# Kernel tuning notes

Measured on AMD Instinct MI355X. Metric: run time of the kernel, lower is better.

The kernel has to match this reference:

```python
import jax, jax.numpy as jnp
import numpy as np

N_NODES = 100000
N_EDGES = 1600000
N_QUERY = 500000
F_IN, HID, EMB = 7, 128, 64


def _glorot(key, fan_in, fan_out):
    lim = float(np.sqrt(6.0 / (fan_in + fan_out)))
    return jax.random.uniform(key, (fan_in, fan_out), jnp.float32, -lim, lim)


def setup_inputs() -> dict:
    key = jax.random.key(0)
    ks = jax.random.split(key, 16)
    x = jax.random.normal(ks[0], (N_NODES, F_IN), jnp.float32)
    edge_index = jax.random.randint(ks[1], (2, N_EDGES), 0, N_NODES, jnp.int64)
    query_edges = jax.random.randint(ks[2], (2, N_QUERY), 0, N_NODES, jnp.int64)
    return {
        "x": x,
        "edge_index": edge_index,
        "query_edges": query_edges,
        # GCN layer 1 / 2
        "W1": _glorot(ks[3], F_IN, HID), "b1": jnp.zeros((HID,), jnp.float32),
        "W2": _glorot(ks[4], HID, HID), "b2": jnp.zeros((HID,), jnp.float32),
        # encoder fc
        "Wfc": _glorot(ks[5], HID, EMB), "bfc": jnp.zeros((EMB,), jnp.float32),
        # decoder MLP
        "Wd1": _glorot(ks[6], 2 * EMB, HID), "bd1": jnp.zeros((HID,), jnp.float32),
        "Wd2": _glorot(ks[7], HID, HID // 2), "bd2": jnp.zeros((HID // 2,), jnp.float32),
        "Wd3": _glorot(ks[8], HID // 2, 1), "bd3": jnp.zeros((1,), jnp.float32),
    }


def _gcn_conv(x, W, b, src, dst, n_nodes):
    """PyG GCNConv: add self-loops + symmetric deg^{-1/2} normalization."""
    h = x @ W  # [N, F_out]
    deg = jnp.ones((n_nodes,), h.dtype).at[dst].add(jnp.ones_like(dst, h.dtype))  # +1 self-loop
    dinv = jax.lax.rsqrt(deg)
    norm = dinv[src] * dinv[dst]  # [E]
    agg = jnp.zeros_like(h).at[dst].add(h[src] * norm[:, None])  # scatter-add messages
    agg = agg + h * (dinv * dinv)[:, None]  # self-loop contribution
    return agg + b


def reference(x, edge_index, query_edges, W1, b1, W2, b2, Wfc, bfc, Wd1, bd1, Wd2, bd2, Wd3, bd3):
    n = x.shape[0]
    src, dst = edge_index[0], edge_index[1]
    # encoder (eval mode: dropout = identity)
    h = jax.nn.relu(_gcn_conv(x, W1, b1, src, dst, n))
    h = jax.nn.relu(_gcn_conv(h, W2, b2, src, dst, n))
    z = h @ Wfc + bfc  # [N, EMB]
    # pair gather + MLP decode
    zc = jnp.concatenate([z[query_edges[0]], z[query_edges[1]]], axis=-1)  # [Q, 2*EMB]
    d = jax.nn.relu(zc @ Wd1 + bd1)
    d = jax.nn.relu(d @ Wd2 + bd2)
    logits = (d @ Wd3 + bd3).squeeze(-1)  # [Q]
    return jax.nn.sigmoid(logits)
```

## Files before the change

### kernel.cpp

```cpp
#include <hip/hip_runtime.h>
#include <hip/hip_bf16.h>
#include <cstdint>
#include <cstddef>

constexpr int TPB = 256;
constexpr int SCAN_B = 1024;
constexpr int NB   = 128;
constexpr int BSH  = 10;
constexpr int NPB  = 1 << BSH;
constexpr int EPB  = 4096;
using bf16x8 = __attribute__((ext_vector_type(8))) short;
using f32x4  = __attribute__((ext_vector_type(4))) float;

static inline int cdiv(int a, int b) { return (a + b - 1) / b; }

__device__ __forceinline__ float bf2f(short u) {
  return __uint_as_float(((unsigned int)(unsigned short)u) << 16);
}
__device__ __forceinline__ short f2bf(float f) {
  unsigned int u = __float_as_uint(f);
  return (short)((u + 0x7FFF + ((u >> 16) & 1)) >> 16);
}


__global__ __launch_bounds__(256)
void bucket_hist_kernel(const int* __restrict__ dst, int* __restrict__ bh,
                        int e_cnt, int n_blk) {
  __shared__ int h[NB];
  int tid = threadIdx.x;
  if (tid < NB) h[tid] = 0;
  __syncthreads();
  int base = blockIdx.x * EPB;
  for (int i = tid; i < EPB; i += TPB) {
    int e = base + i;
    if (e < e_cnt) atomicAdd(&h[dst[e] >> BSH], 1);
  }
  __syncthreads();
  if (tid < NB) bh[tid * n_blk + blockIdx.x] = h[tid];
}

__global__ __launch_bounds__(SCAN_B)
void scan_block_kernel(const int* __restrict__ counts, int* __restrict__ rowptr,
                       int* __restrict__ bsum, int n) {
  __shared__ int wsum[16];
  const int tid = threadIdx.x;
  const int i = blockIdx.x * SCAN_B + tid;
  const int lane = tid & 63;
  const int w = tid >> 6;
  int v = (i < n) ? counts[i] : 0;
  int s = v;
  #pragma unroll
  for (int off = 1; off < 64; off <<= 1) {
    int t = __shfl_up(s, off, 64);
    if (lane >= off) s += t;
  }
  if (lane == 63) wsum[w] = s;
  __syncthreads();
  if (tid < 16) {
    int ws_ = wsum[tid];
    #pragma unroll
    for (int off = 1; off < 16; off <<= 1) {
      int t = __shfl_up(ws_, off, 64);
      if (tid >= off) ws_ += t;
    }
    wsum[tid] = ws_;
  }
  __syncthreads();
  int woff = (w == 0) ? 0 : wsum[w - 1];
  if (i < n) rowptr[i] = woff + s - v;
  if (tid == SCAN_B - 1) bsum[blockIdx.x] = woff + s;
}

__global__ __launch_bounds__(256)
void scan_fin_kernel(int* __restrict__ rowptr, const int* __restrict__ bsum,
                     int nb, int n, int total) {
  __shared__ int sb[128];
  int tid = threadIdx.x;
  if (tid == 0) {
    int run = 0;
    for (int b = 0; b < nb; ++b) { sb[b] = run; run += bsum[b]; }
  }
  __syncthreads();
  int i = blockIdx.x * TPB + tid;
  if (i < n) rowptr[i] += sb[i / SCAN_B];
  if (i == 0) rowptr[n] = total;
}

__global__ __launch_bounds__(256)
void bucket_scatter_kernel(const int* __restrict__ src, const int* __restrict__ dst,
                           const int* __restrict__ eoff, unsigned int* __restrict__ ebuf,
                           int e_cnt, int n_blk) {
  __shared__ int cur[NB];
  int tid = threadIdx.x;
  if (tid < NB) cur[tid] = eoff[tid * n_blk + blockIdx.x];
  __syncthreads();
  int base = blockIdx.x * EPB;
  for (int i = tid; i < EPB; i += TPB) {
    int e = base + i;
    if (e < e_cnt) {
      int d = dst[e];
      int b = d >> BSH;
      int pos = atomicAdd(&cur[b], 1);
      ebuf[pos] = ((unsigned int)src[e] << BSH) | (unsigned int)(d & (NPB - 1));
    }
  }
}

__global__ __launch_bounds__(256)
void node_hist_kernel(const unsigned int* __restrict__ ebuf, const int* __restrict__ eoff,
                      int* __restrict__ counts, float* __restrict__ dinv,
                      int n_blk, int n_nodes) {
  __shared__ int nh[NPB];
  int b = blockIdx.x;
  for (int i = threadIdx.x; i < NPB; i += TPB) nh[i] = 0;
  __syncthreads();
  int wb = eoff[b * n_blk];
  int we = eoff[(b + 1) * n_blk];
  for (int i = wb + threadIdx.x; i < we; i += TPB)
    atomicAdd(&nh[ebuf[i] & (NPB - 1)], 1);
  __syncthreads();
  int nbase = b << BSH;
  for (int i = threadIdx.x; i < NPB; i += TPB) {
    int node = nbase + i;
    if (node < n_nodes) {
      counts[node] = nh[i];
      dinv[node] = rsqrtf((float)nh[i] + 1.0f);
    }
  }
}

__global__ __launch_bounds__(256)
void final_scatter_kernel(const unsigned int* __restrict__ ebuf, const int* __restrict__ eoff,
                          const int* __restrict__ rowptr, int* __restrict__ csr_src,
                          int n_blk, int n_nodes) {
  __shared__ int cur[NPB];
  int b = blockIdx.x;
  int nbase = b << BSH;
  for (int i = threadIdx.x; i < NPB; i += TPB) {
    int node = nbase + i;
    cur[i] = (node < n_nodes) ? rowptr[node] : 0;
  }
  __syncthreads();
  int wb = eoff[b * n_blk];
  int we = eoff[(b + 1) * n_blk];
  for (int i = wb + threadIdx.x; i < we; i += TPB) {
    unsigned int p = ebuf[i];
    int pos = atomicAdd(&cur[p & (NPB - 1)], 1);
    csr_src[pos] = (int)(p >> BSH);
  }
}


__global__ void pad_x8_kernel(const float* __restrict__ x, float* __restrict__ x8, int n) {
  int i = blockIdx.x * TPB + threadIdx.x;
  if (i >= n * 8) return;
  int node = i >> 3, f = i & 7;
  x8[i] = (f < 7) ? x[node * 7 + f] : 0.0f;
}

__global__ __launch_bounds__(256)
void prep_weights_kernel(const float* __restrict__ W1, const float* __restrict__ W2,
                         const float* __restrict__ Wfc, const float* __restrict__ bfc,
                         const float* __restrict__ Wd1, const float* __restrict__ bd1,
                         float* __restrict__ W1p, unsigned short* __restrict__ W2T,
                         unsigned short* __restrict__ WcaT, unsigned short* __restrict__ WcbT,
                         float* __restrict__ bca, float* __restrict__ bcb) {
  int b = blockIdx.x;
  int tid = threadIdx.x;
  if (b == 0) {
    for (int i = tid; i < 8 * 128; i += TPB)
      W1p[i] = (i < 7 * 128) ? W1[i] : 0.0f;
    int j = tid & 127;
    int which = tid >> 7;
    float acc = which ? 0.0f : bd1[j];
    int mo = which ? 64 : 0;
    #pragma unroll 8
    for (int m = 0; m < 64; ++m) acc = fmaf(bfc[m], Wd1[(mo + m) * 128 + j], acc);
    if (which) bcb[j] = acc; else bca[j] = acc;
  } else if (b <= 64) {
    int idx = (b - 1) * 256 + tid;
    int n = idx >> 7, k = idx & 127;
    W2T[idx] = (unsigned short)f2bf(W2[k * 128 + n]);
  } else {
    int idx = (b - 65) * 256 + tid;
    int j = idx >> 7, k = idx & 127;
    float accA = 0.0f, accB = 0.0f;
    #pragma unroll 8
    for (int m = 0; m < 64; ++m) {
      float w = Wfc[k * 64 + m];
      accA = fmaf(w, Wd1[m * 128 + j], accA);
      accB = fmaf(w, Wd1[(64 + m) * 128 + j], accB);
    }
    WcaT[j * 128 + k] = (unsigned short)f2bf(accA);
    WcbT[j * 128 + k] = (unsigned short)f2bf(accB);
  }
}


__global__ __launch_bounds__(256)
void agg_x_kernel(const int* __restrict__ rowptr, const int* __restrict__ csr_src,
                  const float* __restrict__ dinv, const float* __restrict__ x8,
                  float* __restrict__ aggx, int n_nodes) {
  int gid = blockIdx.x * TPB + threadIdx.x;
  int node = gid >> 3;
  int f = gid & 7;
  if (node >= n_nodes) return;
  float dn = dinv[node];
  float acc0 = x8[(size_t)node * 8 + f] * dn * dn;
  float acc1 = 0.0f;
  int beg = rowptr[node], end = rowptr[node + 1];
  int i = beg;
  for (; i + 1 < end; i += 2) {
    int s0 = csr_src[i];
    int s1 = csr_src[i + 1];
    float w0 = dinv[s0] * dn;
    float w1 = dinv[s1] * dn;
    acc0 = fmaf(x8[(size_t)s0 * 8 + f], w0, acc0);
    acc1 = fmaf(x8[(size_t)s1 * 8 + f], w1, acc1);
  }
  if (i < end) {
    int s = csr_src[i];
    acc0 = fmaf(x8[(size_t)s * 8 + f], dinv[s] * dn, acc0);
  }
  aggx[(size_t)node * 8 + f] = acc0 + acc1;
}

__global__ __launch_bounds__(256)
void gather4_kernel(const int* __restrict__ rowptr, const int* __restrict__ csr_src,
                    const float* __restrict__ dinv, const uint4* __restrict__ h1s,
                    uint4* __restrict__ g1, int n_nodes) {
  int wid = (blockIdx.x * TPB + threadIdx.x) >> 6;
  if (wid >= n_nodes) return;
  int lane = threadIdx.x & 63;
  int qtr = lane >> 4;
  int l = lane & 15;
  float acc[8];
  #pragma unroll
  for (int j = 0; j < 8; ++j) acc[j] = 0.0f;
  auto addv = [&](uint4 v) {
    unsigned int u[4] = {v.x, v.y, v.z, v.w};
    #pragma unroll
    for (int p = 0; p < 4; ++p) {
      acc[2 * p]     += __uint_as_float(u[p] << 16);
      acc[2 * p + 1] += __uint_as_float(u[p] & 0xffff0000u);
    }
  };
  if (qtr == 0) addv(h1s[(size_t)wid * 16 + l]);
  int beg = rowptr[wid], end = rowptr[wid + 1];
  int i = beg + qtr;
  for (; i + 4 < end; i += 8) {
    int s0 = csr_src[i];
    int s1 = csr_src[i + 4];
    uint4 v0 = h1s[(size_t)s0 * 16 + l];
    uint4 v1 = h1s[(size_t)s1 * 16 + l];
    addv(v0);
    addv(v1);
  }
  if (i < end) addv(h1s[(size_t)csr_src[i] * 16 + l]);
  #pragma unroll
  for (int j = 0; j < 8; ++j) {
    acc[j] += __shfl_xor(acc[j], 16, 64);
    acc[j] += __shfl_xor(acc[j], 32, 64);
  }
  if (qtr == 0) {
    float dn = dinv[wid];
    unsigned int w[4];
    #pragma unroll
    for (int p = 0; p < 4; ++p) {
      unsigned int lo = (unsigned int)(unsigned short)f2bf(acc[2 * p] * dn);
      unsigned int hi = (unsigned int)(unsigned short)f2bf(acc[2 * p + 1] * dn);
      w[p] = lo | (hi << 16);
    }
    uint4 o; o.x = w[0]; o.y = w[1]; o.z = w[2]; o.w = w[3];
    g1[(size_t)wid * 16 + l] = o;
  }
}

template<int K, int CO>
__global__ __launch_bounds__(256)
void mm_tiled(const float* __restrict__ in, const float* __restrict__ W,
              const float* __restrict__ bias, const float* __restrict__ scale,
              unsigned short* __restrict__ outv, int n_rows) {
  constexpr int BM = 64;
  constexpr int BK = K;
  constexpr int SS = BK + 1 + (BK & 1);
  constexpr int TM = 4;
  constexpr int TN = CO / 16;
  __shared__ float s_in[BM][SS];
  __shared__ float s_w[BK][CO];
  const int tid = threadIdx.x;
  const int base = blockIdx.x * BM;
  const int tr = tid >> 4;
  const int tc = tid & 15;

  float acc[TM][TN];
  #pragma unroll
  for (int m = 0; m < TM; ++m)
    #pragma unroll
    for (int n = 0; n < TN; ++n) acc[m][n] = 0.0f;

  {
    constexpr int F4 = BM * (BK / 4);
    #pragma unroll
    for (int t = tid; t < F4; t += TPB) {
      int r = t / (BK / 4), c4 = t % (BK / 4);
      int row = base + r;
      float4 v = make_float4(0.f, 0.f, 0.f, 0.f);
      if (row < n_rows) v = *(const float4*)(in + (size_t)row * K + c4 * 4);
      s_in[r][c4 * 4 + 0] = v.x;
      s_in[r][c4 * 4 + 1] = v.y;
      s_in[r][c4 * 4 + 2] = v.z;
      s_in[r][c4 * 4 + 3] = v.w;
    }
    constexpr int WF4 = BK * CO / 4;
    #pragma unroll
    for (int t = tid; t < WF4; t += TPB)
      *(float4*)(&s_w[0][0] + t * 4) = *(const float4*)(W + t * 4);
  }
  __syncthreads();

  #pragma unroll
  for (int kk = 0; kk < BK; ++kk) {
    float a[TM], b[TN];
    #pragma unroll
    for (int m = 0; m < TM; ++m) a[m] = s_in[tr * TM + m][kk];
    #pragma unroll
    for (int n = 0; n < TN; ++n) b[n] = s_w[kk][tc + 16 * n];
    #pragma unroll
    for (int m = 0; m < TM; ++m)
      #pragma unroll
      for (int n = 0; n < TN; ++n) acc[m][n] = fmaf(a[m], b[n], acc[m][n]);
  }

  #pragma unroll
  for (int m = 0; m < TM; ++m) {
    int row = base + tr * TM + m;
    if (row < n_rows) {
      float sc = scale[row];
      #pragma unroll
      for (int n = 0; n < TN; ++n) {
        int j = tc + 16 * n;
        float v = fmaxf(acc[m][n] + bias[j], 0.0f) * sc;
        outv[(size_t)row * CO + j] = (unsigned short)f2bf(v);
      }
    }
  }
}

template<int K, int N>
__global__ __launch_bounds__(256)
void mm_mfma(const unsigned short* __restrict__ A, const unsigned short* __restrict__ WT,
             const float* __restrict__ bias, unsigned short* __restrict__ out,
             int n_rows, int do_relu) {
  constexpr int KS = K / 32;
  constexpr int NT = N / 16;
  const int lane = threadIdx.x & 63;
  const int col = lane & 15;
  const int sub = lane >> 4;
  const int wid = threadIdx.x >> 6;

  bf16x8 bfrag[KS][NT];
  #pragma unroll
  for (int ks = 0; ks < KS; ++ks)
    #pragma unroll
    for (int nt = 0; nt < NT; ++nt)
      bfrag[ks][nt] = *(const bf16x8*)(WT + (size_t)(nt * 16 + col) * K + ks * 32 + sub * 8);
  float bv[NT];
  #pragma unroll
  for (int nt = 0; nt < NT; ++nt) bv[nt] = bias ? bias[nt * 16 + col] : 0.0f;

  int ntiles = (n_rows + 15) >> 4;
  int stride = gridDim.x * 4;
  for (int tile = blockIdx.x * 4 + wid; tile < ntiles; tile += stride) {
    int row_a = tile * 16 + col;
    if (row_a >= n_rows) row_a = n_rows - 1;
    bf16x8 afrag[KS];
    #pragma unroll
    for (int ks = 0; ks < KS; ++ks)
      afrag[ks] = *(const bf16x8*)(A + (size_t)row_a * K + ks * 32 + sub * 8);
    f32x4 acc[NT];
    #pragma unroll
    for (int nt = 0; nt < NT; ++nt) acc[nt] = {0.f, 0.f, 0.f, 0.f};
    #pragma unroll
    for (int ks = 0; ks < KS; ++ks)
      #pragma unroll
      for (int nt = 0; nt < NT; ++nt)
        acc[nt] = __builtin_amdgcn_mfma_f32_16x16x32_bf16(afrag[ks], bfrag[ks][nt], acc[nt], 0, 0, 0);
    #pragma unroll
    for (int r = 0; r < 4; ++r) {
      int ro = tile * 16 + sub * 4 + r;
      if (ro < n_rows) {
        #pragma unroll
        for (int nt = 0; nt < NT; ++nt) {
          float v = acc[nt][r] + bv[nt];
          if (do_relu) v = fmaxf(v, 0.0f);
          out[(size_t)ro * N + nt * 16 + col] = (unsigned short)f2bf(v);
        }
      }
    }
  }
}

__global__ __launch_bounds__(256)
void decoder_mfma_kernel(const int* __restrict__ qsrc, const int* __restrict__ qdst,
                         const unsigned short* __restrict__ atab,
                         const unsigned short* __restrict__ btab,
                         const float* __restrict__ Wd2, const float* __restrict__ bd2,
                         const float* __restrict__ Wd3, const float* __restrict__ bd3,
                         float* __restrict__ out, int n_query) {
  const int lane = threadIdx.x & 63;
  const int col = lane & 15;
  const int sub = lane >> 4;

  bf16x8 bfrag[4][4];
  #pragma unroll
  for (int ks = 0; ks < 4; ++ks)
    #pragma unroll
    for (int nt = 0; nt < 4; ++nt) {
      bf16x8 f;
      #pragma unroll
      for (int j = 0; j < 8; ++j) {
        int k = ks * 32 + sub * 8 + j;
        int n = nt * 16 + col;
        f[j] = f2bf(Wd2[k * 64 + n]);
      }
      bfrag[ks][nt] = f;
    }
  float bd2v[4], wd3v[4];
  #pragma unroll
  for (int nt = 0; nt < 4; ++nt) {
    bd2v[nt] = bd2[nt * 16 + col];
    wd3v[nt] = Wd3[nt * 16 + col];
  }
  const float bd3s = bd3[0];

  int wave = (blockIdx.x * TPB + threadIdx.x) >> 6;
  int nwaves = gridDim.x * (TPB / 64);
  int ntiles = (n_query + 15) >> 4;
  for (int t = wave; t < ntiles; t += nwaves) {
    int qb = t << 4;
    int q = qb + col;
    if (q >= n_query) q = n_query - 1;
    int si = qsrc[q], di = qdst[q];
    const bf16x8* ar = (const bf16x8*)(atab + (size_t)si * 128);
    const bf16x8* br = (const bf16x8*)(btab + (size_t)di * 128);
    bf16x8 afrag[4];
    #pragma unroll
    for (int ks = 0; ks < 4; ++ks) {
      bf16x8 av = ar[ks * 4 + sub];
      bf16x8 bv = br[ks * 4 + sub];
      bf16x8 d;
      #pragma unroll
      for (int j = 0; j < 8; ++j)
        d[j] = f2bf(fmaxf(bf2f(av[j]) + bf2f(bv[j]), 0.0f));
      afrag[ks] = d;
    }
    f32x4 acc[4];
    #pragma unroll
    for (int nt = 0; nt < 4; ++nt) acc[nt] = {0.f, 0.f, 0.f, 0.f};
    #pragma unroll
    for (int ks = 0; ks < 4; ++ks)
      #pragma unroll
      for (int nt = 0; nt < 4; ++nt)
        acc[nt] = __builtin_amdgcn_mfma_f32_16x16x32_bf16(afrag[ks], bfrag[ks][nt], acc[nt], 0, 0, 0);
    float part[4] = {0.f, 0.f, 0.f, 0.f};
    #pragma unroll
    for (int nt = 0; nt < 4; ++nt)
      #pragma unroll
      for (int r = 0; r < 4; ++r) {
        float v = fmaxf(acc[nt][r] + bd2v[nt], 0.0f);
        part[r] = fmaf(v, wd3v[nt], part[r]);
      }
    #pragma unroll
    for (int off = 1; off < 16; off <<= 1)
      #pragma unroll
      for (int r = 0; r < 4; ++r) part[r] += __shfl_xor(part[r], off, 64);
    if (col == 0) {
      int row0 = qb + sub * 4;
      #pragma unroll
      for (int r = 0; r < 4; ++r) {
        int qq = row0 + r;
        if (qq < n_query) out[qq] = 1.0f / (1.0f + __expf(-(part[r] + bd3s)));
      }
    }
  }
}

extern "C" void kernel_launch(void* const* d_in, const int* in_sizes, int n_in,
                              void* d_out, int out_size, void* d_ws, size_t ws_size,
                              hipStream_t stream) {
  const float* x    = (const float*)d_in[0];
  const int*   ei   = (const int*)d_in[1];
  const int*   qe   = (const int*)d_in[2];
  const float* W1   = (const float*)d_in[3];
  const float* b1   = (const float*)d_in[4];
  const float* W2   = (const float*)d_in[5];
  const float* b2   = (const float*)d_in[6];
  const float* Wfc  = (const float*)d_in[7];
  const float* bfc  = (const float*)d_in[8];
  const float* Wd1  = (const float*)d_in[9];
  const float* bd1  = (const float*)d_in[10];
  const float* Wd2  = (const float*)d_in[11];
  const float* bd2  = (const float*)d_in[12];
  const float* Wd3  = (const float*)d_in[13];
  const float* bd3  = (const float*)d_in[14];
  float* out = (float*)d_out;

  const int n_nodes = in_sizes[0] / 7;
  const int n_edges = in_sizes[1] / 2;
  const int n_query = in_sizes[2] / 2;
  const int* e_src = ei;
  const int* e_dst = ei + n_edges;
  const int* q_src = qe;
  const int* q_dst = qe + n_query;

  const int n_blk1 = cdiv(n_edges, EPB);
  const int bh_len = NB * n_blk1;
  const int n_bucket = cdiv(n_nodes, NPB);

  char* wp = (char*)d_ws;
  auto take = [&](size_t bytes) { char* p = wp; wp += (bytes + 255) & ~size_t(255); return p; };
  float* dinv    = (float*)take((size_t)n_nodes * 4);
  int*   counts  = (int*)  take((size_t)n_nodes * 4);
  int*   rowptr  = (int*)  take((size_t)(n_nodes + 1) * 4);
  int*   bsum    = (int*)  take(512 * 4);
  int*   bh      = (int*)  take((size_t)(bh_len + 1) * 4);
  int*   eoff    = (int*)  take((size_t)(bh_len + 1) * 4);
  unsigned int* ebuf = (unsigned int*)take((size_t)n_edges * 4);
  int*   csr_src = (int*)  take((size_t)n_edges * 4);
  float* x8      = (float*)take((size_t)n_nodes * 8 * 4);
  float* aggx    = (float*)take((size_t)n_nodes * 8 * 4);
  float* W1p     = (float*)take(8 * 128 * 4);
  unsigned short* W2T   = (unsigned short*)take(128 * 128 * 2);
  unsigned short* WcaT  = (unsigned short*)take(128 * 128 * 2);
  unsigned short* WcbT  = (unsigned short*)take(128 * 128 * 2);
  float* bca     = (float*)take(128 * 4);
  float* bcb     = (float*)take(128 * 4);
  float* bufP    = (float*)take((size_t)n_nodes * 128 * 4);
  float* bufQ    = (float*)take((size_t)n_nodes * 128 * 4);
  float* bufR    = (float*)take((size_t)n_nodes * 64 * 4);

  const int mm_blocks = cdiv(n_nodes, 64);
  const int node_blocks = cdiv(n_nodes, TPB);
  const int scan_blocks = cdiv(n_nodes, SCAN_B);
  const int escan_blocks = cdiv(bh_len, SCAN_B);
  const int mfma_blocks = min(1024, cdiv(cdiv(n_nodes, 16), 4));

  bucket_hist_kernel<<<n_blk1, TPB, 0, stream>>>(e_dst, bh, n_edges, n_blk1);
  scan_block_kernel<<<escan_blocks, SCAN_B, 0, stream>>>(bh, eoff, bsum, bh_len);
  scan_fin_kernel<<<cdiv(bh_len, TPB), TPB, 0, stream>>>(eoff, bsum, escan_blocks, bh_len, n_edges);
  bucket_scatter_kernel<<<n_blk1, TPB, 0, stream>>>(e_src, e_dst, eoff, ebuf, n_edges, n_blk1);
  node_hist_kernel<<<n_bucket, TPB, 0, stream>>>(ebuf, eoff, counts, dinv, n_blk1, n_nodes);
  scan_block_kernel<<<scan_blocks, SCAN_B, 0, stream>>>(counts, rowptr, bsum, n_nodes);
  scan_fin_kernel<<<node_blocks, TPB, 0, stream>>>(rowptr, bsum, scan_blocks, n_nodes, n_edges);
  final_scatter_kernel<<<n_bucket, TPB, 0, stream>>>(ebuf, eoff, rowptr, csr_src, n_blk1, n_nodes);

  pad_x8_kernel<<<cdiv(n_nodes * 8, TPB), TPB, 0, stream>>>(x, x8, n_nodes);
  prep_weights_kernel<<<129, TPB, 0, stream>>>(W1, W2, Wfc, bfc, Wd1, bd1,
                                               W1p, W2T, WcaT, WcbT, bca, bcb);

  agg_x_kernel<<<cdiv(n_nodes * 8, TPB), TPB, 0, stream>>>(rowptr, csr_src, dinv, x8, aggx, n_nodes);
  mm_tiled<8, 128><<<mm_blocks, TPB, 0, stream>>>(aggx, W1p, b1, dinv, (unsigned short*)bufP, n_nodes);

  gather4_kernel<<<cdiv(n_nodes * 64, TPB), TPB, 0, stream>>>(rowptr, csr_src, dinv,
                                                              (const uint4*)bufP, (uint4*)bufQ, n_nodes);
  mm_mfma<128, 128><<<mfma_blocks, TPB, 0, stream>>>((const unsigned short*)bufQ, W2T, b2,
                                                     (unsigned short*)bufP, n_nodes, 1);

  unsigned short* atab = (unsigned short*)bufQ;
  unsigned short* btab = (unsigned short*)bufR;
  mm_mfma<128, 128><<<mfma_blocks, TPB, 0, stream>>>((const unsigned short*)bufP, WcaT, bca,
                                                     atab, n_nodes, 0);
  mm_mfma<128, 128><<<mfma_blocks, TPB, 0, stream>>>((const unsigned short*)bufP, WcbT, bcb,
                                                     btab, n_nodes, 0);

  decoder_mfma_kernel<<<2048, TPB, 0, stream>>>(q_src, q_dst, atab, btab, Wd2, bd2, Wd3, bd3, out, n_query);
}
```

Before: 306.0 us.

## Fuse layer-2 neighbor gather with W2 MFMA matmul; drop x padding kernel

Replaces the separate layer-2 gather kernel and its MFMA matmul with one fused kernel. Each block aggregates 64 nodes into shared-memory bf16 rows, then multiplies them by W2 (staged in padded LDS) using MFMA. This avoids writing and re-reading the intermediate aggregated features through global memory and saves a kernel launch. The pad_x8 kernel is also removed, with agg_x reading the unpadded 7-wide x directly. Each wave now processes 16 nodes serially, and the per-block W2 staging lowers parallelism and may reduce occupancy.

Measured after the change: 370.6 us. +21.1%, slower.

```diff
diff --git a/kernel.cpp b/kernel.cpp
--- a/kernel.cpp
+++ b/kernel.cpp
@@ -9,6 +9,7 @@
 constexpr int BSH  = 10;
 constexpr int NPB  = 1 << BSH;
 constexpr int EPB  = 4096;
+constexpr int LP   = 136;
 using bf16x8 = __attribute__((ext_vector_type(8))) short;
 using f32x4  = __attribute__((ext_vector_type(4))) float;
 
@@ -150,13 +151,6 @@
   }
 }
 
-
-__global__ void pad_x8_kernel(const float* __restrict__ x, float* __restrict__ x8, int n) {
-  int i = blockIdx.x * TPB + threadIdx.x;
-  if (i >= n * 8) return;
-  int node = i >> 3, f = i & 7;
-  x8[i] = (f < 7) ? x[node * 7 + f] : 0.0f;
-}
 
 __global__ __launch_bounds__(256)
 void prep_weights_kernel(const float* __restrict__ W1, const float* __restrict__ W2,
@@ -199,14 +193,15 @@
 
 __global__ __launch_bounds__(256)
 void agg_x_kernel(const int* __restrict__ rowptr, const int* __restrict__ csr_src,
-                  const float* __restrict__ dinv, const float* __restrict__ x8,
+                  const float* __restrict__ dinv, const float* __restrict__ x,
                   float* __restrict__ aggx, int n_nodes) {
   int gid = blockIdx.x * TPB + threadIdx.x;
   int node = gid >> 3;
   int f = gid & 7;
   if (node >= n_nodes) return;
+  bool live = (f < 7);
   float dn = dinv[node];
-  float acc0 = x8[(size_t)node * 8 + f] * dn * dn;
+  float acc0 = live ? x[(size_t)node * 7 + f] * dn * dn : 0.0f;
   float acc1 = 0.0f;
   int beg = rowptr[node], end = rowptr[node + 1];
   int i = beg;
@@ -215,65 +210,16 @@
     int s1 = csr_src[i + 1];
     float w0 = dinv[s0] * dn;
     float w1 = dinv[s1] * dn;
-    acc0 = fmaf(x8[(size_t)s0 * 8 + f], w0, acc0);
-    acc1 = fmaf(x8[(size_t)s1 * 8 + f], w1, acc1);
-  }
-  if (i < end) {
+    if (live) {
+      acc0 = fmaf(x[(size_t)s0 * 7 + f], w0, acc0);
+      acc1 = fmaf(x[(size_t)s1 * 7 + f], w1, acc1);
+    }
+  }
+  if (i < end && live) {
     int s = csr_src[i];
-    acc0 = fmaf(x8[(size_t)s * 8 + f], dinv[s] * dn, acc0);
+    acc0 = fmaf(x[(size_t)s * 7 + f], dinv[s] * dn, acc0);
   }
   aggx[(size_t)node * 8 + f] = acc0 + acc1;
-}
-
-__global__ __launch_bounds__(256)
-void gather4_kernel(const int* __restrict__ rowptr, const int* __restrict__ csr_src,
-                    const float* __restrict__ dinv, const uint4* __restrict__ h1s,
-                    uint4* __restrict__ g1, int n_nodes) {
-  int wid = (blockIdx.x * TPB + threadIdx.x) >> 6;
-  if (wid >= n_nodes) return;
-  int lane = threadIdx.x & 63;
-  int qtr = lane >> 4;
-  int l = lane & 15;
-  float acc[8];
-  #pragma unroll
-  for (int j = 0; j < 8; ++j) acc[j] = 0.0f;
-  auto addv = [&](uint4 v) {
-    unsigned int u[4] = {v.x, v.y, v.z, v.w};
-    #pragma unroll
-    for (int p = 0; p < 4; ++p) {
-      acc[2 * p]     += __uint_as_float(u[p] << 16);
-      acc[2 * p + 1] += __uint_as_float(u[p] & 0xffff0000u);
-    }
-  };
-  if (qtr == 0) addv(h1s[(size_t)wid * 16 + l]);
-  int beg = rowptr[wid], end = rowptr[wid + 1];
-  int i = beg + qtr;
-  for (; i + 4 < end; i += 8) {
-    int s0 = csr_src[i];
-    int s1 = csr_src[i + 4];
-    uint4 v0 = h1s[(size_t)s0 * 16 + l];
-    uint4 v1 = h1s[(size_t)s1 * 16 + l];
-    addv(v0);
-    addv(v1);
-  }
-  if (i < end) addv(h1s[(size_t)csr_src[i] * 16 + l]);
-  #pragma unroll
-  for (int j = 0; j < 8; ++j) {
-    acc[j] += __shfl_xor(acc[j], 16, 64);
-    acc[j] += __shfl_xor(acc[j], 32, 64);
-  }
-  if (qtr == 0) {
-    float dn = dinv[wid];
-    unsigned int w[4];
-    #pragma unroll
-    for (int p = 0; p < 4; ++p) {
-      unsigned int lo = (unsigned int)(unsigned short)f2bf(acc[2 * p] * dn);
-      unsigned int hi = (unsigned int)(unsigned short)f2bf(acc[2 * p + 1] * dn);
-      w[p] = lo | (hi << 16);
-    }
-    uint4 o; o.x = w[0]; o.y = w[1]; o.z = w[2]; o.w = w[3];
-    g1[(size_t)wid * 16 + l] = o;
-  }
 }
 
 template<int K, int CO>
@@ -342,6 +288,98 @@
         int j = tc + 16 * n;
         float v = fmaxf(acc[m][n] + bias[j], 0.0f) * sc;
         outv[(size_t)row * CO + j] = (unsigned short)f2bf(v);
+      }
+    }
+  }
+}
+
+__global__ __launch_bounds__(256)
+void gcn_fused_kernel(const int* __restrict__ rowptr, const int* __restrict__ csr_src,
+                      const float* __restrict__ dinv, const uint4* __restrict__ h1s,
+                      const unsigned short* __restrict__ W2T, const float* __restrict__ b2,
+                      unsigned short* __restrict__ h2, int n_nodes) {
+  __shared__ unsigned short g1s[64 * LP];
+  __shared__ unsigned short w2s[128 * LP];
+  const int tid = threadIdx.x;
+  for (int i = tid; i < 128 * 16; i += TPB) {
+    int row = i >> 4, seg = i & 15;
+    *(uint4*)&w2s[row * LP + seg * 8] = *(const uint4*)(W2T + (size_t)row * 128 + seg * 8);
+  }
+  __syncthreads();
+
+  const int lane = tid & 63;
+  const int w = tid >> 6;
+  const int qtr = lane >> 4;
+  const int l = lane & 15;
+  const int base = blockIdx.x * 64;
+
+  for (int nn = 0; nn < 16; ++nn) {
+    int node = base + w * 16 + nn;
+    if (node >= n_nodes) break;
+    float acc[8];
+    #pragma unroll
+    for (int j = 0; j < 8; ++j) acc[j] = 0.0f;
+    auto addv = [&](uint4 v) {
+      unsigned int u[4] = {v.x, v.y, v.z, v.w};
+      #pragma unroll
+      for (int p = 0; p < 4; ++p) {
+        acc[2 * p]     += __uint_as_float(u[p] << 16);
+        acc[2 * p + 1] += __uint_as_float(u[p] & 0xffff0000u);
+      }
+    };
+    if (qtr == 0) addv(h1s[(size_t)node * 16 + l]);
+    int beg = rowptr[node], end = rowptr[node + 1];
+    int i = beg + qtr;
+    for (; i + 4 < end; i += 8) {
+      int s0 = csr_src[i];
+      int s1 = csr_src[i + 4];
+      uint4 v0 = h1s[(size_t)s0 * 16 + l];
+      uint4 v1 = h1s[(size_t)s1 * 16 + l];
+      addv(v0);
+      addv(v1);
+    }
+    if (i < end) addv(h1s[(size_t)csr_src[i] * 16 + l]);
+    #pragma unroll
+    for (int j = 0; j < 8; ++j) {
+      acc[j] += __shfl_xor(acc[j], 16, 64);
+      acc[j] += __shfl_xor(acc[j], 32, 64);
+    }
+    if (qtr == 0) {
+      float dn = dinv[node];
+      unsigned int wv[4];
+      #pragma unroll
+      for (int p = 0; p < 4; ++p) {
+        unsigned int lo = (unsigned int)(unsigned short)f2bf(acc[2 * p] * dn);
+        unsigned int hi = (unsigned int)(unsigned short)f2bf(acc[2 * p + 1] * dn);
+        wv[p] = lo | (hi << 16);
+      }
+      uint4 o; o.x = wv[0]; o.y = wv[1]; o.z = wv[2]; o.w = wv[3];
+      *(uint4*)&g1s[(w * 16 + nn) * LP + l * 8] = o;
+    }
+  }
+
+  bf16x8 afrag[4];
+  #pragma unroll
+  for (int ks = 0; ks < 4; ++ks)
+    afrag[ks] = *(const bf16x8*)&g1s[(w * 16 + l) * LP + ks * 32 + qtr * 8];
+  f32x4 acc[8];
+  #pragma unroll
+  for (int nt = 0; nt < 8; ++nt) acc[nt] = {0.f, 0.f, 0.f, 0.f};
+  #pragma unroll
+  for (int ks = 0; ks < 4; ++ks)
+    #pragma unroll
+    for (int nt = 0; nt < 8; ++nt) {
+      bf16x8 bfrag = *(const bf16x8*)&w2s[(nt * 16 + l) * LP + ks * 32 + qtr * 8];
+      acc[nt] = __builtin_amdgcn_mfma_f32_16x16x32_bf16(afrag[ks], bfrag, acc[nt], 0, 0, 0);
+    }
+  #pragma unroll
+  for (int r = 0; r < 4; ++r) {
+    int node = base + w * 16 + qtr * 4 + r;
+    if (node < n_nodes) {
+      #pragma unroll
+      for (int nt = 0; nt < 8; ++nt) {
+        float v = fmaxf(acc[nt][r] + b2[nt * 16 + l], 0.0f);
+        h2[(size_t)node * 128 + nt * 16 + l] = (unsigned short)f2bf(v);
       }
     }
   }
@@ -528,7 +566,6 @@
   int*   eoff    = (int*)  take((size_t)(bh_len + 1) * 4);
   unsigned int* ebuf = (unsigned int*)take((size_t)n_edges * 4);
   int*   csr_src = (int*)  take((size_t)n_edges * 4);
-  float* x8      = (float*)take((size_t)n_nodes * 8 * 4);
   float* aggx    = (float*)take((size_t)n_nodes * 8 * 4);
   float* W1p     = (float*)take(8 * 128 * 4);
   unsigned short* W2T   = (unsigned short*)take(128 * 128 * 2);
@@ -555,23 +592,21 @@
   scan_fin_kernel<<<node_blocks, TPB, 0, stream>>>(rowptr, bsum, scan_blocks, n_nodes, n_edges);
   final_scatter_kernel<<<n_bucket, TPB, 0, stream>>>(ebuf, eoff, rowptr, csr_src, n_blk1, n_nodes);
 
-  pad_x8_kernel<<<cdiv(n_nodes * 8, TPB), TPB, 0, stream>>>(x, x8, n_nodes);
   prep_weights_kernel<<<129, TPB, 0, stream>>>(W1, W2, Wfc, bfc, Wd1, bd1,
                                                W1p, W2T, WcaT, WcbT, bca, bcb);
 
-  agg_x_kernel<<<cdiv(n_nodes * 8, TPB), TPB, 0, stream>>>(rowptr, csr_src, dinv, x8, aggx, n_nodes);
+  agg_x_kernel<<<cdiv(n_nodes * 8, TPB), TPB, 0, stream>>>(rowptr, csr_src, dinv, x, aggx, n_nodes);
   mm_tiled<8, 128><<<mm_blocks, TPB, 0, stream>>>(aggx, W1p, b1, dinv, (unsigned short*)bufP, n_nodes);
 
-  gather4_kernel<<<cdiv(n_nodes * 64, TPB), TPB, 0, stream>>>(rowptr, csr_src, dinv,
-                                                              (const uint4*)bufP, (uint4*)bufQ, n_nodes);
-  mm_mfma<128, 128><<<mfma_blocks, TPB, 0, stream>>>((const unsigned short*)bufQ, W2T, b2,
-                                                     (unsigned short*)bufP, n_nodes, 1);
-
-  unsigned short* atab = (unsigned short*)bufQ;
+  gcn_fused_kernel<<<cdiv(n_nodes, 64), TPB, 0, stream>>>(rowptr, csr_src, dinv,
+                                                          (const uint4*)bufP, W2T, b2,
+                                                          (unsigned short*)bufQ, n_nodes);
+
+  unsigned short* atab = (unsigned short*)bufP;
   unsigned short* btab = (unsigned short*)bufR;
-  mm_mfma<128, 128><<<mfma_blocks, TPB, 0, stream>>>((const unsigned short*)bufP, WcaT, bca,
+  mm_mfma<128, 128><<<mfma_blocks, TPB, 0, stream>>>((const unsigned short*)bufQ, WcaT, bca,
                                                      atab, n_nodes, 0);
-  mm_mfma<128, 128><<<mfma_blocks, TPB, 0, stream>>>((const unsigned short*)bufP, WcbT, bcb,
+  mm_mfma<128, 128><<<mfma_blocks, TPB, 0, stream>>>((const unsigned short*)bufQ, WcbT, bcb,
                                                      btab, n_nodes, 0);
 
   decoder_mfma_kernel<<<2048, TPB, 0, stream>>>(q_src, q_dst, atab, btab, Wd2, bd2, Wd3, bd3, out, n_query);
```
